# Kernel optimization log

Hardware: AMD Instinct MI355X
Metric: run time of the kernel (lower is better)

Reference implementation:

```python
import jax, jax.numpy as jnp
import numpy as np

N_SRC = 20000
N_TAR = 20000
DIM = 3


def setup_inputs() -> dict:
    key = jax.random.key(0)
    k1, k2 = jax.random.split(key)
    src_V = jax.random.normal(k1, (N_SRC, DIM), dtype=jnp.float32)
    tar_V = jax.random.normal(k2, (N_TAR, DIM), dtype=jnp.float32)
    return {"src_V": src_V, "tar_V": tar_V}


def reference(src_V, tar_V):
    # Brute-force 1-NN replacing the CPU cKDTree query.
    # Squared distances: ||t||^2 - 2 t.s^T + ||s||^2  -> [M, N]
    d2 = (
        jnp.sum(tar_V * tar_V, axis=1, keepdims=True)
        - 2.0 * (tar_V @ src_V.T)
        + jnp.sum(src_V * src_V, axis=1)[None, :]
    )
    ii = jnp.argmin(d2, axis=1)          # nearest src index per tar point
    diff = src_V[ii] - tar_V             # gather + residual, [M, 3]
    return 0.5 * jnp.sum(diff * diff)
```

## Files before the change

kernel.cpp:

```cpp
#include <hip/hip_runtime.h>
#include <float.h>

#define N_SRC 20000
#define N_TAR 20000
#define TPB 512
#define SPLITS 8
#define PHASES 2
#define TILES 40
#define TGRP 79
#define FBLOCKS ((N_TAR + 255) / 256)

typedef _Float16 half8 __attribute__((ext_vector_type(8)));
typedef float floatx16 __attribute__((ext_vector_type(16)));

__device__ float g_part[SPLITS * N_TAR];

#define ROTMIN(v, ctrl) \
    fminf(v, __int_as_float(__builtin_amdgcn_mov_dpp(__float_as_int(v), ctrl, 0xF, 0xF, false)))

__global__ __launch_bounds__(TPB) void nn_mfma(
    const float* __restrict__ src, const float* __restrict__ tar,
    float* __restrict__ out)
{
    if (blockIdx.x == 0 && blockIdx.y == 0 && threadIdx.x == 0) out[0] = 0.f;

    __shared__ alignas(16) _Float16 lds[TILES * 32 * 16];

    const int tid  = threadIdx.x;
    const int lane = tid & 63;
    const int col  = lane & 31;
    const int hsel = (lane >> 5) & 1;
    const int wave = tid >> 6;

    const int strip = blockIdx.x * 8 + wave;
    const int t = min(strip * 32 + col, N_TAR - 1);
    const float tx = tar[t * 3 + 0];
    const float ty = tar[t * 3 + 1];
    const float tz = tar[t * 3 + 2];
    const _Float16 txh = (_Float16)tx, tyh = (_Float16)ty, tzh = (_Float16)tz;
    const _Float16 txl = (_Float16)(tx - (float)txh);
    const _Float16 tyl = (_Float16)(ty - (float)tyh);
    const _Float16 tzl = (_Float16)(tz - (float)tzh);
    half8 a;
    if (hsel == 0)
        a = (half8){-txh, -tyh, -tzh, -txl, -tyl, -tzl, -txh, -tyh};
    else
        a = (half8){-tzh, (_Float16)1.f, (_Float16)1.f, 0, 0, 0, 0, 0};

    floatx16 m;
#pragma unroll
    for (int i = 0; i < 16; ++i) m[i] = FLT_MAX;
    const floatx16 zero = {};
    const int foff = col * 16 + hsel * 8;
    const int sbase0 = blockIdx.y * (PHASES * TILES * 32);

    for (int phase = 0; phase < PHASES; ++phase) {
        if (phase) __syncthreads();

        const int pbase = sbase0 + phase * (TILES * 32);
        for (int ls = tid; ls < TILES * 32; ls += TPB) {
            const int s = pbase + ls;
            half8 f0 = {0, 0, 0, 0, 0, 0, 0, 0};
            half8 f1 = {0, 0, 0, 0, 0, 0, 0, 0};
            if (s < N_SRC) {
                const float x = src[s * 3 + 0];
                const float y = src[s * 3 + 1];
                const float z = src[s * 3 + 2];
                const _Float16 xh = (_Float16)x, yh = (_Float16)y, zh = (_Float16)z;
                const _Float16 xl = (_Float16)(x - (float)xh);
                const _Float16 yl = (_Float16)(y - (float)yh);
                const _Float16 zl = (_Float16)(z - (float)zh);
                const float nrm = 0.5f * (x * x + y * y + z * z);
                const _Float16 nh = (_Float16)nrm;
                const _Float16 nl = (_Float16)(nrm - (float)nh);
                f0 = (half8){xh, yh, zh, xh, yh, zh, xl, yl};
                f1 = (half8){zl, nh, nl, 0, 0, 0, 0, 0};
            } else {
                f1 = (half8){0, (_Float16)30000.f, 0, 0, 0, 0, 0, 0};
            }
            *(half8*)&lds[ls * 16 + 0] = f0;
            *(half8*)&lds[ls * 16 + 8] = f1;
        }

        __syncthreads();

#pragma unroll 2
        for (int tp = 0; tp < TILES; tp += 2) {
            const half8 b0 = *(const half8*)&lds[tp * 512 + foff];
            const half8 b1 = *(const half8*)&lds[(tp + 1) * 512 + foff];
            const floatx16 d0 = __builtin_amdgcn_mfma_f32_32x32x16_f16(a, b0, zero, 0, 0, 0);
            const floatx16 d1 = __builtin_amdgcn_mfma_f32_32x32x16_f16(a, b1, zero, 0, 0, 0);
#pragma unroll
            for (int i = 0; i < 16; ++i)
                m[i] = fminf(fminf(d0[i], d1[i]), m[i]);
        }
    }

#pragma unroll
    for (int i = 0; i < 16; ++i) {
        float v = m[i];
        v = ROTMIN(v, 0x128);
        v = ROTMIN(v, 0x124);
        v = ROTMIN(v, 0x122);
        v = ROTMIN(v, 0x121);
        m[i] = fminf(v, __shfl_xor(v, 16));
    }
    if (col == 0) {
#pragma unroll
        for (int i = 0; i < 16; ++i) {
            const int row = (i & 3) + 8 * (i >> 2) + 4 * hsel;
            const int tt = min(strip * 32 + row, N_TAR - 1);
            g_part[blockIdx.y * N_TAR + tt] = m[i];
        }
    }
}

__global__ __launch_bounds__(256) void nn_finalize(
    const float* __restrict__ tar, float* __restrict__ out)
{
    const int t = blockIdx.x * 256 + threadIdx.x;
    float contrib = 0.f;
    if (t < N_TAR) {
        float m = FLT_MAX;
#pragma unroll
        for (int c = 0; c < SPLITS; ++c) m = fminf(m, g_part[c * N_TAR + t]);
        const float tx = tar[t * 3 + 0];
        const float ty = tar[t * 3 + 1];
        const float tz = tar[t * 3 + 2];
        contrib = 0.5f * (tx * tx + ty * ty + tz * tz) + m;
    }
    for (int off = 32; off > 0; off >>= 1)
        contrib += __shfl_down(contrib, off);
    __shared__ float red[4];
    if ((threadIdx.x & 63) == 0) red[threadIdx.x >> 6] = contrib;
    __syncthreads();
    if (threadIdx.x == 0) {
        float s = 0.f;
#pragma unroll
        for (int w = 0; w < 4; ++w) s += red[w];
        atomicAdd(out, s);
    }
}

extern "C" void kernel_launch(void* const* d_in, const int* in_sizes, int n_in,
                              void* d_out, int out_size, void* d_ws, size_t ws_size,
                              hipStream_t stream) {
    const float* src = (const float*)d_in[0];
    const float* tar = (const float*)d_in[1];
    float* out = (float*)d_out;
    (void)d_ws; (void)ws_size;

    dim3 grid1(TGRP, SPLITS);
    nn_mfma<<<grid1, TPB, 0, stream>>>(src, tar, out);
    nn_finalize<<<FBLOCKS, 256, 0, stream>>>(tar, out);
}
```

Baseline: 75.77 us.

## Fuse finalize reduction into MFMA kernel via last-arriving-block completion counter

Removes the second kernel launch by having the last 40 blocks to finish (counted with a global atomic counter) spin-wait until all blocks have written their partial minima, then perform the per-target min-over-splits and sum reduction. This is meant to cut the launch gap and tail of the separate finalize kernel. In exchange it adds a grid-wide spin-wait on a persistent counter, which needs all blocks to be co-resident or to finish first. It also keeps the out[0] zeroing race from block (0,0) against finalizers' atomicAdds.

```diff
diff --git a/kernel.cpp b/kernel.cpp
--- a/kernel.cpp
+++ b/kernel.cpp
@@ -8,23 +8,28 @@
 #define PHASES 2
 #define TILES 40
 #define TGRP 79
-#define FBLOCKS ((N_TAR + 255) / 256)
+#define NBLK (TGRP * SPLITS)
+#define NFIN 40
+#define TPERF (N_TAR / NFIN)
 
 typedef _Float16 half8 __attribute__((ext_vector_type(8)));
 typedef float floatx16 __attribute__((ext_vector_type(16)));
 
 __device__ float g_part[SPLITS * N_TAR];
+__device__ unsigned g_done = 0;
 
 #define ROTMIN(v, ctrl) \
     fminf(v, __int_as_float(__builtin_amdgcn_mov_dpp(__float_as_int(v), ctrl, 0xF, 0xF, false)))
 
-__global__ __launch_bounds__(TPB) void nn_mfma(
+__global__ __launch_bounds__(TPB) void nn_fused(
     const float* __restrict__ src, const float* __restrict__ tar,
     float* __restrict__ out)
 {
     if (blockIdx.x == 0 && blockIdx.y == 0 && threadIdx.x == 0) out[0] = 0.f;
 
     __shared__ alignas(16) _Float16 lds[TILES * 32 * 16];
+    __shared__ int fidx;
+    __shared__ float red[8];
 
     const int tid  = threadIdx.x;
     const int lane = tid & 63;
@@ -113,31 +118,45 @@
             g_part[blockIdx.y * N_TAR + tt] = m[i];
         }
     }
-}
 
-__global__ __launch_bounds__(256) void nn_finalize(
-    const float* __restrict__ tar, float* __restrict__ out)
-{
-    const int t = blockIdx.x * 256 + threadIdx.x;
-    float contrib = 0.f;
-    if (t < N_TAR) {
-        float m = FLT_MAX;
+    __syncthreads();
+    if (tid == 0) {
+        const unsigned old = __hip_atomic_fetch_add(&g_done, 1u, __ATOMIC_RELEASE,
+                                                    __HIP_MEMORY_SCOPE_AGENT);
+        const unsigned pos = old % NBLK;
+        int f = (int)pos - (NBLK - NFIN);
+        if (f >= 0) {
+            const unsigned goal = (old / NBLK + 1u) * NBLK;
+            while (__hip_atomic_load(&g_done, __ATOMIC_RELAXED,
+                                     __HIP_MEMORY_SCOPE_AGENT) < goal)
+                __builtin_amdgcn_s_sleep(8);
+            __threadfence();
+        }
+        fidx = f;
+    }
+    __syncthreads();
+    if (fidx < 0) return;
+
+    const int tbase = fidx * TPERF;
+    float local = 0.f;
+    for (int k = tid; k < TPERF; k += TPB) {
+        const int tt = tbase + k;
+        float mn = FLT_MAX;
 #pragma unroll
-        for (int c = 0; c < SPLITS; ++c) m = fminf(m, g_part[c * N_TAR + t]);
-        const float tx = tar[t * 3 + 0];
-        const float ty = tar[t * 3 + 1];
-        const float tz = tar[t * 3 + 2];
-        contrib = 0.5f * (tx * tx + ty * ty + tz * tz) + m;
+        for (int c = 0; c < SPLITS; ++c) mn = fminf(mn, g_part[c * N_TAR + tt]);
+        const float x = tar[tt * 3 + 0];
+        const float y = tar[tt * 3 + 1];
+        const float z = tar[tt * 3 + 2];
+        local += 0.5f * (x * x + y * y + z * z) + mn;
     }
     for (int off = 32; off > 0; off >>= 1)
-        contrib += __shfl_down(contrib, off);
-    __shared__ float red[4];
-    if ((threadIdx.x & 63) == 0) red[threadIdx.x >> 6] = contrib;
+        local += __shfl_down(local, off);
+    if ((tid & 63) == 0) red[tid >> 6] = local;
     __syncthreads();
-    if (threadIdx.x == 0) {
+    if (tid == 0) {
         float s = 0.f;
 #pragma unroll
-        for (int w = 0; w < 4; ++w) s += red[w];
+        for (int w = 0; w < 8; ++w) s += red[w];
         atomicAdd(out, s);
     }
 }
@@ -150,7 +169,6 @@
     float* out = (float*)d_out;
     (void)d_ws; (void)ws_size;
 
-    dim3 grid1(TGRP, SPLITS);
-    nn_mfma<<<grid1, TPB, 0, stream>>>(src, tar, out);
-    nn_finalize<<<FBLOCKS, 256, 0, stream>>>(tar, out);
+    dim3 grid(TGRP, SPLITS);
+    nn_fused<<<grid, TPB, 0, stream>>>(src, tar, out);
 }
```

New measurement: 93.14 us. +22.9%, slower.

## Prefetch second source phase into registers and rebalance source splits to ten

Applied to the files above, without the earlier changes.

The global loads for the second source tile are now issued into registers before the first phase's MFMA loop runs, so their latency can overlap with compute. The first phase's loads are also issued before the target setup. The source dimension is split ten ways with 2000 points per split and 32 tiles per phase instead of 8 splits of 40 tiles. This raises the block count and cuts LDS per block, at the cost of a small redundant overlap of 48 sources between adjacent splits and more partial minima to reduce in the finalize kernel.

```diff
diff --git a/kernel.cpp b/kernel.cpp
--- a/kernel.cpp
+++ b/kernel.cpp
@@ -4,9 +4,10 @@
 #define N_SRC 20000
 #define N_TAR 20000
 #define TPB 512
-#define SPLITS 8
+#define SPLITS 10
 #define PHASES 2
-#define TILES 40
+#define TILES 32
+#define SRC_PER_SPLIT 2000
 #define TGRP 79
 #define FBLOCKS ((N_TAR + 255) / 256)
 
@@ -17,6 +18,38 @@
 
 #define ROTMIN(v, ctrl) \
     fminf(v, __int_as_float(__builtin_amdgcn_mov_dpp(__float_as_int(v), ctrl, 0xF, 0xF, false)))
+
+struct SrcReg { float x, y, z; bool ok; };
+
+__device__ __forceinline__ SrcReg load_src(const float* __restrict__ src, int s) {
+    SrcReg r;
+    r.ok = (s < N_SRC);
+    const int sc = r.ok ? s : 0;
+    r.x = src[sc * 3 + 0];
+    r.y = src[sc * 3 + 1];
+    r.z = src[sc * 3 + 2];
+    return r;
+}
+
+__device__ __forceinline__ void cvt_store(_Float16* lds, int ls, SrcReg r) {
+    half8 f0 = {0, 0, 0, 0, 0, 0, 0, 0};
+    half8 f1;
+    if (r.ok) {
+        const _Float16 xh = (_Float16)r.x, yh = (_Float16)r.y, zh = (_Float16)r.z;
+        const _Float16 xl = (_Float16)(r.x - (float)xh);
+        const _Float16 yl = (_Float16)(r.y - (float)yh);
+        const _Float16 zl = (_Float16)(r.z - (float)zh);
+        const float nrm = 0.5f * (r.x * r.x + r.y * r.y + r.z * r.z);
+        const _Float16 nh = (_Float16)nrm;
+        const _Float16 nl = (_Float16)(nrm - (float)nh);
+        f0 = (half8){xh, yh, zh, xh, yh, zh, xl, yl};
+        f1 = (half8){zl, nh, nl, 0, 0, 0, 0, 0};
+    } else {
+        f1 = (half8){0, (_Float16)30000.f, 0, 0, 0, 0, 0, 0};
+    }
+    *(half8*)&lds[ls * 16 + 0] = f0;
+    *(half8*)&lds[ls * 16 + 8] = f1;
+}
 
 __global__ __launch_bounds__(TPB) void nn_mfma(
     const float* __restrict__ src, const float* __restrict__ tar,
@@ -31,6 +64,11 @@
     const int col  = lane & 31;
     const int hsel = (lane >> 5) & 1;
     const int wave = tid >> 6;
+
+    const int sbase = blockIdx.y * SRC_PER_SPLIT;
+
+    SrcReg s0a = load_src(src, sbase + tid);
+    SrcReg s0b = load_src(src, sbase + tid + TPB);
 
     const int strip = blockIdx.x * 8 + wave;
     const int t = min(strip * 32 + col, N_TAR - 1);
@@ -47,53 +85,44 @@
     else
         a = (half8){-tzh, (_Float16)1.f, (_Float16)1.f, 0, 0, 0, 0, 0};
 
+    cvt_store(lds, tid, s0a);
+    cvt_store(lds, tid + TPB, s0b);
+    __syncthreads();
+
+    SrcReg s1a = load_src(src, sbase + TILES * 32 + tid);
+    SrcReg s1b = load_src(src, sbase + TILES * 32 + tid + TPB);
+
     floatx16 m;
 #pragma unroll
     for (int i = 0; i < 16; ++i) m[i] = FLT_MAX;
     const floatx16 zero = {};
     const int foff = col * 16 + hsel * 8;
-    const int sbase0 = blockIdx.y * (PHASES * TILES * 32);
-
-    for (int phase = 0; phase < PHASES; ++phase) {
-        if (phase) __syncthreads();
-
-        const int pbase = sbase0 + phase * (TILES * 32);
-        for (int ls = tid; ls < TILES * 32; ls += TPB) {
-            const int s = pbase + ls;
-            half8 f0 = {0, 0, 0, 0, 0, 0, 0, 0};
-            half8 f1 = {0, 0, 0, 0, 0, 0, 0, 0};
-            if (s < N_SRC) {
-                const float x = src[s * 3 + 0];
-                const float y = src[s * 3 + 1];
-                const float z = src[s * 3 + 2];
-                const _Float16 xh = (_Float16)x, yh = (_Float16)y, zh = (_Float16)z;
-                const _Float16 xl = (_Float16)(x - (float)xh);
-                const _Float16 yl = (_Float16)(y - (float)yh);
-                const _Float16 zl = (_Float16)(z - (float)zh);
-                const float nrm = 0.5f * (x * x + y * y + z * z);
-                const _Float16 nh = (_Float16)nrm;
-                const _Float16 nl = (_Float16)(nrm - (float)nh);
-                f0 = (half8){xh, yh, zh, xh, yh, zh, xl, yl};
-                f1 = (half8){zl, nh, nl, 0, 0, 0, 0, 0};
-            } else {
-                f1 = (half8){0, (_Float16)30000.f, 0, 0, 0, 0, 0, 0};
-            }
-            *(half8*)&lds[ls * 16 + 0] = f0;
-            *(half8*)&lds[ls * 16 + 8] = f1;
-        }
-
-        __syncthreads();
 
 #pragma unroll 2
-        for (int tp = 0; tp < TILES; tp += 2) {
-            const half8 b0 = *(const half8*)&lds[tp * 512 + foff];
-            const half8 b1 = *(const half8*)&lds[(tp + 1) * 512 + foff];
-            const floatx16 d0 = __builtin_amdgcn_mfma_f32_32x32x16_f16(a, b0, zero, 0, 0, 0);
-            const floatx16 d1 = __builtin_amdgcn_mfma_f32_32x32x16_f16(a, b1, zero, 0, 0, 0);
+    for (int tp = 0; tp < TILES; tp += 2) {
+        const half8 b0 = *(const half8*)&lds[tp * 512 + foff];
+        const half8 b1 = *(const half8*)&lds[(tp + 1) * 512 + foff];
+        const floatx16 d0 = __builtin_amdgcn_mfma_f32_32x32x16_f16(a, b0, zero, 0, 0, 0);
+        const floatx16 d1 = __builtin_amdgcn_mfma_f32_32x32x16_f16(a, b1, zero, 0, 0, 0);
 #pragma unroll
-            for (int i = 0; i < 16; ++i)
-                m[i] = fminf(fminf(d0[i], d1[i]), m[i]);
-        }
+        for (int i = 0; i < 16; ++i)
+            m[i] = fminf(fminf(d0[i], d1[i]), m[i]);
+    }
+
+    __syncthreads();
+    cvt_store(lds, tid, s1a);
+    cvt_store(lds, tid + TPB, s1b);
+    __syncthreads();
+
+#pragma unroll 2
+    for (int tp = 0; tp < TILES; tp += 2) {
+        const half8 b0 = *(const half8*)&lds[tp * 512 + foff];
+        const half8 b1 = *(const half8*)&lds[(tp + 1) * 512 + foff];
+        const floatx16 d0 = __builtin_amdgcn_mfma_f32_32x32x16_f16(a, b0, zero, 0, 0, 0);
+        const floatx16 d1 = __builtin_amdgcn_mfma_f32_32x32x16_f16(a, b1, zero, 0, 0, 0);
+#pragma unroll
+        for (int i = 0; i < 16; ++i)
+            m[i] = fminf(fminf(d0[i], d1[i]), m[i]);
     }
 
 #pragma unroll
```

Measured after the change: 77.81 us. 1.03x slower.
